# Performance work log

Measured on AMD Instinct MI355X. Metric: run time of the kernel, lower is better.

The kernel has to match this reference:

```python
import jax, jax.numpy as jnp
import numpy as np

D = 128  # chunk_embSize

def _mlp_one_layer(x, W, b):
    # MLP_one_layer in eval mode: dropout is identity -> tanh(x @ W^T + b)
    return jnp.tanh(x @ W.T + b)

def setup_inputs() -> dict:
    key = jax.random.key(0)
    ks = jax.random.split(key, 10)
    n_item, n_opi, n_user, L = 50000, 5000, 10000, 50
    s = 0.02  # initializer_range-style scale for linear weights
    return {
        "item_table": jax.random.normal(ks[0], (n_item, D), jnp.float32),
        "opin_table": jax.random.normal(ks[1], (n_opi, D), jnp.float32),
        "user_emb": jax.random.normal(ks[2], (n_user, D), jnp.float32),
        "attr_embedding": jax.random.normal(ks[3], (D,), jnp.float32),
        "Wq": jax.random.normal(ks[4], (D, D), jnp.float32) * s,
        "bq": jnp.zeros((D,), jnp.float32),
        "Wk": jax.random.normal(ks[5], (D, D), jnp.float32) * s,
        "bk": jnp.zeros((D,), jnp.float32),
        "Wv": jax.random.normal(ks[6], (D, D), jnp.float32) * s,
        "bv": jnp.zeros((D,), jnp.float32),
        "item_seqs": jax.random.randint(ks[7], (n_user, L), 0, n_item, jnp.int64),
        "opin_seqs": jax.random.randint(ks[8], (n_user, L), 0, n_opi, jnp.int64),
    }

def reference(item_table, opin_table, user_emb, attr_embedding,
              Wq, bq, Wk, bk, Wv, bv, item_seqs, opin_seqs):
    # FineRec UiMatrix.opin_update_ui (eval mode: all dropouts identity)
    item_emb = item_table[item_seqs]          # [U, L, D] gather
    opin_emb = opin_table[opin_seqs]          # [U, L, D] gather
    # k = k_layer(attr + item); v = v_layer(item + opin); q = q_layer(user)
    k_emb = _mlp_one_layer(attr_embedding[None, None, :] + item_emb, Wk, bk)
    v_emb = _mlp_one_layer(item_emb + opin_emb, Wv, bv)
    q_emb = _mlp_one_layer(user_emb, Wq, bq)  # [U, D]
    # unnormalized attention weights over the user's interaction sequence
    w_agg = jnp.einsum("ud,uld->ul", q_emb, k_emb)  # [U, L]
    mask = (item_seqs > 0).astype(w_agg.dtype)       # padding mask
    w_agg = w_agg * mask
    # weighted aggregation over sequence -> new user embedding
    user_embedding = jnp.einsum("ul,uld->ud", w_agg, v_emb)  # [U, D]
    return user_embedding
```

## Files before the change

kernel.cpp:

```cpp
#include <hip/hip_runtime.h>
#include <hip/hip_bf16.h>
#include <stdint.h>

typedef __attribute__((ext_vector_type(8))) short bf16x8;
typedef __attribute__((ext_vector_type(4))) float f32x4;

#define S_2LOG2E 2.8853900817779268f

#if __has_builtin(__builtin_amdgcn_exp2f)
#define EXP2F(x) __builtin_amdgcn_exp2f(x)
#else
#define EXP2F(x) __expf((x) * 0.6931471805599453f)
#endif
#if __has_builtin(__builtin_amdgcn_rcpf)
#define RCPF(x) __builtin_amdgcn_rcpf(x)
#else
#define RCPF(x) (1.0f / (x))
#endif

__device__ __forceinline__ float tanh_z(float z) {
    float e = EXP2F(z);
    float r = RCPF(e + 1.0f);
    return fmaf(-2.0f, r, 1.0f);
}
__device__ __forceinline__ float tanh_fast(float x) {
    float e = __expf(2.0f * x);
    return 1.0f - 2.0f / (e + 1.0f);
}

__device__ __forceinline__ bf16x8 pack2(float4 a, float4 b) {
    union { bf16x8 v; __hip_bfloat162 h[4]; } r;
    r.h[0] = __float22bfloat162_rn(make_float2(a.x, a.y));
    r.h[1] = __float22bfloat162_rn(make_float2(a.z, a.w));
    r.h[2] = __float22bfloat162_rn(make_float2(b.x, b.y));
    r.h[3] = __float22bfloat162_rn(make_float2(b.z, b.w));
    return r.v;
}
__device__ __forceinline__ float4 scl4(float4 a) {
    a.x *= S_2LOG2E; a.y *= S_2LOG2E; a.z *= S_2LOG2E; a.w *= S_2LOG2E;
    return a;
}
#define MFMA16(a, b, c) __builtin_amdgcn_mfma_f32_16x16x32_bf16((a), (b), (c), 0, 0, 0)

__global__ void finerec_prep(
    const float* __restrict__ user_emb, const float* __restrict__ attr,
    const float* __restrict__ Wq, const float* __restrict__ bq,
    const float* __restrict__ Wk, const float* __restrict__ bk,
    const float* __restrict__ Wv, const float* __restrict__ bv,
    const float* __restrict__ item_table, const float* __restrict__ opin_table,
    float* __restrict__ q_ws, float* __restrict__ bkz_ws, float* __restrict__ bvz_ws,
    short* __restrict__ wf_ws, short* __restrict__ itb, short* __restrict__ opb,
    float* __restrict__ out, int U, int n_item, int n_opi, int qb)
{
    const int bx = blockIdx.x, tid = threadIdx.x;
    if (bx >= qb + 49) {
        const int castb = gridDim.x - qb - 49;
        const int gid = (bx - qb - 49) * 256 + tid;
        const int stride = castb * 256;
        const int tci = n_item * 16, tc = (n_item + n_opi) * 16;
        for (int c = gid; c < tc; c += stride) {
            if (c < tci) {
                const float* src = item_table + (size_t)c * 8;
                ((bf16x8*)itb)[c] = pack2(*(const float4*)src, *(const float4*)(src + 4));
            } else {
                const float* src = opin_table + (size_t)(c - tci) * 8;
                ((bf16x8*)opb)[c - tci] = pack2(*(const float4*)src, *(const float4*)(src + 4));
            }
        }
        return;
    }
    if (bx >= qb + 9) {
        const int gid = (bx - qb - 9) * 256 + tid;
        float4 z = {0.0f, 0.0f, 0.0f, 0.0f};
        for (int i = gid; i < U * 32; i += 40 * 256) ((float4*)out)[i] = z;
        return;
    }
    if (bx >= qb + 1) {
        const int bi = bx - qb - 1;
#pragma unroll
        for (int t = 0; t < 2; ++t) {
            const int g = bi * 512 + t * 256 + tid;
            const int mat = g >> 11, gg = g & 2047, r = gg >> 4, c = gg & 15;
            const float* src = (mat ? Wv : Wk) + r * 128 + c * 8;
            ((bf16x8*)wf_ws)[(mat << 11) + (r << 4) + (c ^ (r & 15))] =
                pack2(scl4(*(const float4*)src), scl4(*(const float4*)(src + 4)));
        }
        return;
    }
    if (bx == qb) {
        if (tid < 128) {
            const float* wr = Wk + tid * 128;
            float s = bk[tid];
            for (int k = 0; k < 128; k += 4) {
                float4 w4 = *(const float4*)(wr + k);
                float4 a4 = *(const float4*)(attr + k);
                s += w4.x * a4.x + w4.y * a4.y + w4.z * a4.z + w4.w * a4.w;
            }
            bkz_ws[tid] = s * S_2LOG2E;
        } else if (tid < 256) {
            bvz_ws[tid - 128] = bv[tid - 128] * S_2LOG2E;
        }
        return;
    }
    const int wv = tid >> 6, lane = tid & 63;
    const int l15 = lane & 15, quad = lane >> 4;
    const int u0 = (bx * 4 + wv) * 16;
    int ur = u0 + l15; if (ur >= U) ur = U - 1;
    const float* up = user_emb + (size_t)ur * 128 + quad * 8;
    bf16x8 af[4];
#pragma unroll
    for (int ks = 0; ks < 4; ++ks)
        af[ks] = pack2(*(const float4*)(up + ks * 32), *(const float4*)(up + ks * 32 + 4));
#pragma unroll
    for (int nt = 0; nt < 8; ++nt) {
        const int n = nt * 16 + l15;
        const float* wp = Wq + n * 128 + quad * 8;
        f32x4 acc = {0, 0, 0, 0};
#pragma unroll
        for (int ks = 0; ks < 4; ++ks) {
            bf16x8 bf = pack2(*(const float4*)(wp + ks * 32), *(const float4*)(wp + ks * 32 + 4));
            acc = MFMA16(af[ks], bf, acc);
        }
        const float bqv = bq[n];
#pragma unroll
        for (int r = 0; r < 4; ++r) {
            int row = u0 + quad * 4 + r;
            if (row < U) q_ws[row * 128 + nt * 16 + l15] = tanh_fast(acc[r] + bqv);
        }
    }
}

template<int BF16, int LC>
__global__ __launch_bounds__(1024, 4) void finerec_main(
    const float* __restrict__ item_table, const float* __restrict__ opin_table,
    const int* __restrict__ item_seqs, const int* __restrict__ opin_seqs,
    const float* __restrict__ q_ws, const float* __restrict__ bkz_ws,
    const float* __restrict__ bvz_ws, const short* __restrict__ wf_ws,
    const short* __restrict__ itb, const short* __restrict__ opb,
    float* __restrict__ out, int U, int Lrt)
{
    __shared__ __align__(16) short wlds[32768];
    __shared__ float bkz_lds[128], bvz_lds[128];

    const int L = LC ? LC : Lrt;
    const int tid = threadIdx.x;
    const int wv = tid >> 6, lane = tid & 63, l15 = lane & 15, quad = lane >> 4;

    const bf16x8* wsrc = (const bf16x8*)wf_ws;
    bf16x8* wldsv = (bf16x8*)wlds;
#pragma unroll
    for (int i = 0; i < 4; ++i)
        wldsv[i * 1024 + tid] = wsrc[i * 1024 + tid];
    if (tid < 128)      bkz_lds[tid]       = bkz_ws[tid];
    else if (tid < 256) bvz_lds[tid - 128] = bvz_ws[tid - 128];
    __syncthreads();

    const int UL = U * L;
    const int njobs = (UL + 15) >> 4;
    const int nwaves = gridDim.x * 16;

#pragma unroll 1
    for (int job = blockIdx.x * 16 + wv; job < njobs; job += nwaves) {
        const int g0 = job << 4;
        const int uA = g0 / L;
        const int bb = L - (g0 - uA * L);
        const bool split = (bb < 16) && (uA + 1 < U);

        int vi = 0, vo = 0;
        if (lane < 16 && g0 + lane < UL) {
            vi = item_seqs[g0 + lane];
            vo = opin_seqs[g0 + lane];
        }
        const unsigned long long mb = __ballot(vi > 0);

        const int idx = __shfl(vi, l15);
        bf16x8 ai[4];
        if (BF16) {
            const bf16x8* pb = (const bf16x8*)itb + (size_t)idx * 16 + quad;
#pragma unroll
            for (int ks = 0; ks < 4; ++ks) ai[ks] = pb[ks * 4];
        } else {
            const float* p = item_table + (size_t)idx * 128 + quad * 8;
#pragma unroll
            for (int ks = 0; ks < 4; ++ks)
                ai[ks] = pack2(*(const float4*)(p + ks * 32), *(const float4*)(p + ks * 32 + 4));
        }

        const float* qpA = q_ws + (size_t)uA * 128;
        float w[4] = {0, 0, 0, 0};

        if (!split) {
#pragma unroll 1
            for (int nt = 0; nt < 8; ++nt) {
                const int n = nt * 16 + l15;
                const float qa = qpA[n];
                const float bz = bkz_lds[n];
                f32x4 c = {bz, bz, bz, bz};
#pragma unroll
                for (int ks = 0; ks < 4; ++ks)
                    c = MFMA16(ai[ks], wldsv[(n << 4) + ((ks * 4 + quad) ^ l15)], c);
#pragma unroll
                for (int r = 0; r < 4; ++r)
                    w[r] = fmaf(qa, tanh_z(c[r]), w[r]);
            }
        } else {
            const float* qpB = qpA + 128;
#pragma unroll 1
            for (int nt = 0; nt < 8; ++nt) {
                const int n = nt * 16 + l15;
                const float qa = qpA[n];
                const float qb2 = qpB[n];
                const float bz = bkz_lds[n];
                f32x4 c = {bz, bz, bz, bz};
#pragma unroll
                for (int ks = 0; ks < 4; ++ks)
                    c = MFMA16(ai[ks], wldsv[(n << 4) + ((ks * 4 + quad) ^ l15)], c);
#pragma unroll
                for (int r = 0; r < 4; ++r) {
                    const float qv = (quad * 4 + r < bb) ? qa : qb2;
                    w[r] = fmaf(qv, tanh_z(c[r]), w[r]);
                }
            }
        }
#pragma unroll
        for (int r = 0; r < 4; ++r) {
            float t = w[r];
            t += __shfl_xor(t, 1); t += __shfl_xor(t, 2);
            t += __shfl_xor(t, 4); t += __shfl_xor(t, 8);
            w[r] = ((mb >> (quad * 4 + r)) & 1ull) ? t : 0.0f;
        }
        const int od = __shfl(vo, l15);
        bf16x8 ao[4];
        if (BF16) {
            const bf16x8* pb = (const bf16x8*)opb + (size_t)od * 16 + quad;
#pragma unroll
            for (int ks = 0; ks < 4; ++ks) ao[ks] = pb[ks * 4];
        } else {
            const float* p = opin_table + (size_t)od * 128 + quad * 8;
#pragma unroll
            for (int ks = 0; ks < 4; ++ks)
                ao[ks] = pack2(*(const float4*)(p + ks * 32), *(const float4*)(p + ks * 32 + 4));
        }
        float* op = out + (size_t)uA * 128 + quad * 32 + l15;
        if (!split) {
            float s0 = 0.0f, s1 = 0.0f;
#pragma unroll 1
            for (int nt = 0; nt < 8; ++nt) {
                const int n = nt * 16 + l15;
                const float bz = bvz_lds[n];
                f32x4 c = {bz, bz, bz, bz};
#pragma unroll
                for (int ks = 0; ks < 4; ++ks) {
                    const bf16x8 wf = wldsv[2048 + (n << 4) + ((ks * 4 + quad) ^ l15)];
                    c = MFMA16(ai[ks], wf, c);
                    c = MFMA16(ao[ks], wf, c);
                }
                float acc = 0.0f;
#pragma unroll
                for (int r = 0; r < 4; ++r)
                    acc = fmaf(w[r], tanh_z(c[r]), acc);
                acc += __shfl_xor(acc, 16);
                acc += __shfl_xor(acc, 32);
                const bool mine = (quad == (nt >> 1));
                s0 += (mine && !(nt & 1)) ? acc : 0.0f;
                s1 += (mine &&  (nt & 1)) ? acc : 0.0f;
            }
            atomicAdd(op, s0);
            atomicAdd(op + 16, s1);
        } else {
            float sA0 = 0.0f, sA1 = 0.0f, sB0 = 0.0f, sB1 = 0.0f;
#pragma unroll 1
            for (int nt = 0; nt < 8; ++nt) {
                const int n = nt * 16 + l15;
                const float bz = bvz_lds[n];
                f32x4 c = {bz, bz, bz, bz};
#pragma unroll
                for (int ks = 0; ks < 4; ++ks) {
                    const bf16x8 wf = wldsv[2048 + (n << 4) + ((ks * 4 + quad) ^ l15)];
                    c = MFMA16(ai[ks], wf, c);
                    c = MFMA16(ao[ks], wf, c);
                }
                float accT = 0.0f, accA = 0.0f;
#pragma unroll
                for (int r = 0; r < 4; ++r) {
                    const float t = w[r] * tanh_z(c[r]);
                    accT += t;
                    accA += (quad * 4 + r < bb) ? t : 0.0f;
                }
                accT += __shfl_xor(accT, 16); accT += __shfl_xor(accT, 32);
                accA += __shfl_xor(accA, 16); accA += __shfl_xor(accA, 32);
                const float accB = accT - accA;
                const bool mine = (quad == (nt >> 1));
                const bool lo = !(nt & 1);
                sA0 += (mine && lo)  ? accA : 0.0f;
                sA1 += (mine && !lo) ? accA : 0.0f;
                sB0 += (mine && lo)  ? accB : 0.0f;
                sB1 += (mine && !lo) ? accB : 0.0f;
            }
            atomicAdd(op, sA0);
            atomicAdd(op + 16, sA1);
            atomicAdd(op + 128, sB0);
            atomicAdd(op + 144, sB1);
        }
    }
}

extern "C" void kernel_launch(void* const* d_in, const int* in_sizes, int n_in,
                              void* d_out, int out_size, void* d_ws, size_t ws_size,
                              hipStream_t stream) {
    const float* item_table = (const float*)d_in[0];
    const float* opin_table = (const float*)d_in[1];
    const float* user_emb   = (const float*)d_in[2];
    const float* attr       = (const float*)d_in[3];
    const float* Wq = (const float*)d_in[4];
    const float* bq = (const float*)d_in[5];
    const float* Wk = (const float*)d_in[6];
    const float* bk = (const float*)d_in[7];
    const float* Wv = (const float*)d_in[8];
    const float* bv = (const float*)d_in[9];
    const int* item_seqs = (const int*)d_in[10];
    const int* opin_seqs = (const int*)d_in[11];
    float* out = (float*)d_out;

    const int U = in_sizes[2] / 128;
    const int L = in_sizes[10] / U;
    const int n_item = in_sizes[0] / 128;
    const int n_opi  = in_sizes[1] / 128;

    char* w = (char*)d_ws;
    float* q_ws   = (float*)w;               w += (size_t)U * 128 * 4;
    float* bkz_ws = (float*)w;               w += 512;
    float* bvz_ws = (float*)w;               w += 512;
    short* wf_ws  = (short*)w;               w += 4096 * 16;
    short* itb    = (short*)w;               w += (size_t)n_item * 128 * 2;
    short* opb    = (short*)w;               w += (size_t)n_opi * 128 * 2;
    const size_t need = (size_t)(w - (char*)d_ws);
    const int use_bf16 = (ws_size >= need) ? 1 : 0;

    const int qb = (U + 63) / 64;
    const int castb = use_bf16 ? (((n_item + n_opi) * 16 + 255) / 256) : 0;
    const int prep_grid = qb + 49 + castb;
    finerec_prep<<<prep_grid, 256, 0, stream>>>(
        user_emb, attr, Wq, bq, Wk, bk, Wv, bv, item_table, opin_table,
        q_ws, bkz_ws, bvz_ws, wf_ws, itb, opb, out, U, n_item, n_opi, qb);

    if (use_bf16) {
        if (L == 50)
            finerec_main<1, 50><<<512, 1024, 0, stream>>>(
                item_table, opin_table, item_seqs, opin_seqs,
                q_ws, bkz_ws, bvz_ws, wf_ws, itb, opb, out, U, L);
        else
            finerec_main<1, 0><<<512, 1024, 0, stream>>>(
                item_table, opin_table, item_seqs, opin_seqs,
                q_ws, bkz_ws, bvz_ws, wf_ws, itb, opb, out, U, L);
    } else {
        if (L == 50)
            finerec_main<0, 50><<<512, 1024, 0, stream>>>(
                item_table, opin_table, item_seqs, opin_seqs,
                q_ws, bkz_ws, bvz_ws, wf_ws, itb, opb, out, U, L);
        else
            finerec_main<0, 0><<<512, 1024, 0, stream>>>(
                item_table, opin_table, item_seqs, opin_seqs,
                q_ws, bkz_ws, bvz_ws, wf_ws, itb, opb, out, U, L);
    }
}
```

Measured before the change: 179.1 us.

## Pre-add item and opinion bf16 vectors and read V weights from global memory

The V projection now adds the item and opinion embeddings in bf16 before the matmul, using one MFMA per k-step instead of two. That halves the V-layer MFMA work. The V weight matrix is no longer staged in LDS and is read directly from global memory (through cache), which halves the LDS footprint and may allow more resident blocks. The costs are an extra bf16 rounding after the add, and per-iteration global/L2 loads of weight fragments in place of LDS reads.

```diff
diff --git a/kernel.cpp b/kernel.cpp
--- a/kernel.cpp
+++ b/kernel.cpp
@@ -39,6 +39,20 @@
 __device__ __forceinline__ float4 scl4(float4 a) {
     a.x *= S_2LOG2E; a.y *= S_2LOG2E; a.z *= S_2LOG2E; a.w *= S_2LOG2E;
     return a;
+}
+__device__ __forceinline__ bf16x8 bfadd8(bf16x8 a, bf16x8 b) {
+    union { bf16x8 v; unsigned int u[4]; } A, B, R;
+    A.v = a; B.v = b;
+#pragma unroll
+    for (int i = 0; i < 4; ++i) {
+        float al = __uint_as_float(A.u[i] << 16);
+        float ah = __uint_as_float(A.u[i] & 0xffff0000u);
+        float bl = __uint_as_float(B.u[i] << 16);
+        float bh = __uint_as_float(B.u[i] & 0xffff0000u);
+        __hip_bfloat162 p = __float22bfloat162_rn(make_float2(al + bl, ah + bh));
+        R.u[i] = *reinterpret_cast<unsigned int*>(&p);
+    }
+    return R.v;
 }
 #define MFMA16(a, b, c) __builtin_amdgcn_mfma_f32_16x16x32_bf16((a), (b), (c), 0, 0, 0)
 
@@ -139,7 +153,7 @@
     const short* __restrict__ itb, const short* __restrict__ opb,
     float* __restrict__ out, int U, int Lrt)
 {
-    __shared__ __align__(16) short wlds[32768];
+    __shared__ __align__(16) short wlds[16384];
     __shared__ float bkz_lds[128], bvz_lds[128];
 
     const int L = LC ? LC : Lrt;
@@ -147,9 +161,10 @@
     const int wv = tid >> 6, lane = tid & 63, l15 = lane & 15, quad = lane >> 4;
 
     const bf16x8* wsrc = (const bf16x8*)wf_ws;
+    const bf16x8* wsrcV = wsrc + 2048;
     bf16x8* wldsv = (bf16x8*)wlds;
 #pragma unroll
-    for (int i = 0; i < 4; ++i)
+    for (int i = 0; i < 2; ++i)
         wldsv[i * 1024 + tid] = wsrc[i * 1024 + tid];
     if (tid < 128)      bkz_lds[tid]       = bkz_ws[tid];
     else if (tid < 256) bvz_lds[tid - 128] = bvz_ws[tid - 128];
@@ -230,16 +245,17 @@
             w[r] = ((mb >> (quad * 4 + r)) & 1ull) ? t : 0.0f;
         }
         const int od = __shfl(vo, l15);
-        bf16x8 ao[4];
+        bf16x8 av[4];
         if (BF16) {
             const bf16x8* pb = (const bf16x8*)opb + (size_t)od * 16 + quad;
 #pragma unroll
-            for (int ks = 0; ks < 4; ++ks) ao[ks] = pb[ks * 4];
+            for (int ks = 0; ks < 4; ++ks) av[ks] = bfadd8(ai[ks], pb[ks * 4]);
         } else {
             const float* p = opin_table + (size_t)od * 128 + quad * 8;
 #pragma unroll
             for (int ks = 0; ks < 4; ++ks)
-                ao[ks] = pack2(*(const float4*)(p + ks * 32), *(const float4*)(p + ks * 32 + 4));
+                av[ks] = bfadd8(ai[ks],
+                    pack2(*(const float4*)(p + ks * 32), *(const float4*)(p + ks * 32 + 4)));
         }
         float* op = out + (size_t)uA * 128 + quad * 32 + l15;
         if (!split) {
@@ -250,11 +266,8 @@
                 const float bz = bvz_lds[n];
                 f32x4 c = {bz, bz, bz, bz};
 #pragma unroll
-                for (int ks = 0; ks < 4; ++ks) {
-                    const bf16x8 wf = wldsv[2048 + (n << 4) + ((ks * 4 + quad) ^ l15)];
-                    c = MFMA16(ai[ks], wf, c);
-                    c = MFMA16(ao[ks], wf, c);
-                }
+                for (int ks = 0; ks < 4; ++ks)
+                    c = MFMA16(av[ks], wsrcV[(n << 4) + ((ks * 4 + quad) ^ l15)], c);
                 float acc = 0.0f;
 #pragma unroll
                 for (int r = 0; r < 4; ++r)
@@ -275,11 +288,8 @@
                 const float bz = bvz_lds[n];
                 f32x4 c = {bz, bz, bz, bz};
 #pragma unroll
-                for (int ks = 0; ks < 4; ++ks) {
-                    const bf16x8 wf = wldsv[2048 + (n << 4) + ((ks * 4 + quad) ^ l15)];
-                    c = MFMA16(ai[ks], wf, c);
-                    c = MFMA16(ao[ks], wf, c);
-                }
+                for (int ks = 0; ks < 4; ++ks)
+                    c = MFMA16(av[ks], wsrcV[(n << 4) + ((ks * 4 + quad) ^ l15)], c);
                 float accT = 0.0f, accA = 0.0f;
 #pragma unroll
                 for (int r = 0; r < 4; ++r) {
```

New measurement: 205.5 us. +14.7%, slower.
